# Kernel tuning notes

Measured on AMD Instinct MI355X. Metric: run time of the kernel, lower is better.

## Reference

```python
import jax, jax.numpy as jnp
import numpy as np

D = 4          # subsample stride for quantized refs
R = 6          # local search radius
P = 2 * R + 1  # 13
N = P * P      # 169
C = 32         # one-hot classes
BETA = 50.0
SIG = 1.0      # gaussian kernel sigma for kernel_soft_argmax
MPR = 12       # memory_patch_R
MPP = 2 * MPR + 1  # 25
DIL_INT = 15


def bilinear_gather(img, ys, xs):
    # img (b,c,h,w); ys,xs (b,n,h,w) float pixel coords; zero padding outside.
    b, c, h, w = img.shape
    y0f = jnp.floor(ys); x0f = jnp.floor(xs)
    wy = ys - y0f; wx = xs - x0f
    y0 = y0f.astype(jnp.int32); x0 = x0f.astype(jnp.int32)
    imgf = img.reshape(b, c, h * w)

    def corner(yi, xi, wgt):
        valid = (yi >= 0) & (yi < h) & (xi >= 0) & (xi < w)
        idx = jnp.clip(yi, 0, h - 1) * w + jnp.clip(xi, 0, w - 1)  # (b,n,h,w)
        g = jax.vmap(lambda f, ix: f[:, ix])(imgf, idx)            # (b,c,n,h,w)
        return g * (wgt * valid)[:, None]

    return (corner(y0, x0, (1 - wy) * (1 - wx))
            + corner(y0, x0 + 1, (1 - wy) * wx)
            + corner(y0 + 1, x0, wy * (1 - wx))
            + corner(y0 + 1, x0 + 1, wy * wx))


def deform_im2col(img, offset):
    # img (b,c,h,w); offset (b,h,w,2) ordered (dx,dy); returns (b,c,N,h,w)
    b, c, h, w = img.shape
    n = jnp.arange(N)
    dy = (n // P - R).astype(jnp.float32)
    dx = (n % P - R).astype(jnp.float32)
    yy = jnp.arange(h, dtype=jnp.float32)[:, None]
    xx = jnp.arange(w, dtype=jnp.float32)[None, :]
    ys = yy[None, None] + offset[..., 1][:, None] + dy[None, :, None, None]
    xs = xx[None, None] + offset[..., 0][:, None] + dx[None, :, None, None]
    return bilinear_gather(img, ys, xs)


def local_corr(t, r, rad, dil):
    # SpatialCorrelationSampler(kernel_size=1, patch_size=2*rad+1, dilation_patch=dil)
    pad = rad * dil
    rp = jnp.pad(r, ((0, 0), (0, 0), (pad, pad), (pad, pad)))
    offs = jnp.arange(2 * rad + 1) * dil

    def dot(oy, ox):
        rs = jax.lax.dynamic_slice(rp, (0, 0, oy, ox), t.shape)
        return jnp.sum(t * rs, axis=1)  # (b,h,w)

    f = jax.vmap(lambda oy: jax.vmap(lambda ox: dot(oy, ox))(offs))(offs)  # (Pp,Pp,b,h,w)
    return jnp.transpose(f, (2, 0, 1, 3, 4))  # (b,Pp,Pp,h,w), axis1=dy, axis2=dx


def unfold(x, ksz, pad):
    # torch F.unfold: (b,c,h,w) -> (b,c,ksz*ksz,h*w), n = ky*ksz+kx, zero pad
    b, c, h, w = x.shape
    xp = jnp.pad(x, ((0, 0), (0, 0), (pad, pad), (pad, pad)))
    offs = jnp.arange(ksz)
    sl = jax.vmap(lambda oy: jax.vmap(
        lambda ox: jax.lax.dynamic_slice(xp, (0, 0, oy, ox), x.shape))(offs))(offs)
    return jnp.transpose(sl, (2, 3, 0, 1, 4, 5)).reshape(b, c, ksz * ksz, h * w)


def kernel_soft_argmax(corr):
    # corr (B, N, h, w): gaussian-weight then softmax(beta * .) over N
    k = jnp.arange(P, dtype=jnp.float32)
    ctr = (P - 1) / 2.0
    g = jnp.exp(-(((k[None, :] - ctr) ** 2) + ((k[:, None] - ctr) ** 2)) / (2 * SIG ** 2))
    return jax.nn.softmax(BETA * (g.reshape(1, N, 1, 1) * corr), axis=1)


def get_grid(corr):
    # corr (B, N, h, w) -> soft-argmax grid (B, h, w, 2) in normalized coords
    B, n, h, w = corr.shape
    # replicate the torch meshgrid variable swap in the original get_grid
    x_map = jnp.broadcast_to(jnp.linspace(-1.0, 1.0, w)[None, :], (h, w)).astype(jnp.float32)
    y_map = jnp.broadcast_to(jnp.linspace(-1.0, 1.0, h)[:, None], (h, w)).astype(jnp.float32)
    xg = unfold(x_map[None, None], P, R)[:, 0]  # (1,N,hw)
    yg = unfold(y_map[None, None], P, R)[:, 0]
    wgt = corr.reshape(B, n, h * w)
    wgt = wgt / jnp.sum(wgt, 1, keepdims=True)
    gx = (wgt * xg).sum(1).reshape(B, h, w, 1)
    gy = (wgt * yg).sum(1).reshape(B, h, w, 1)
    return jnp.concatenate([gx, gy], 3)


def forward(feats_r, feats_t, quantized_r, ref_index, current_ind):
    ref_list = [int(v) for v in np.asarray(ref_index)]  # static config
    cur = int(current_ind)
    nref = feats_r.shape[0]
    nsearch = len([x for x in ref_list if cur - x > DIL_INT])
    dirates = [min(4, (cur - x) // DIL_INT + 1) for x in ref_list if cur - x > DIL_INT]
    b, c, h, w = feats_t.shape

    mdy = jnp.arange(-MPR, MPR + 1, dtype=jnp.float32)
    corrs, offsets = [], []
    for si in range(nsearch):
        cc = local_corr(feats_t, feats_r[si], MPR, dirates[si])       # (b,25,25,h,w)
        cc = jax.nn.softmax(cc.reshape(b, MPP * MPP, h * w), axis=1)
        cc = cc.reshape(b, MPP, MPP, h, w)
        offx = jnp.einsum('bpqhw,q->bhw', cc, mdy)   # expectation of dx
        offy = jnp.einsum('bpqhw,p->bhw', cc, mdy)   # expectation of dy
        off = jnp.stack([offx, offy], -1) * float(dirates[si])        # (b,h,w,2)
        offsets.append(off)
        col0 = deform_im2col(feats_r[si], off)                        # (b,c,N,h,w)
        corrs.append(jnp.einsum('bchw,bcnhw->bnhw', feats_t, col0))
    for ind in range(nsearch, nref):
        corrs.append(local_corr(feats_t, feats_r[ind], R, 1).reshape(b, N, h, w))

    corr = jnp.concatenate(corrs, 0)                 # (b*nref, N, h, w)
    corr = kernel_soft_argmax(corr)
    corr = corr.reshape(b, 1, N * nref, h * w)
    grid = get_grid(corr.reshape(-1, N, h, w))       # (b*nref, h, w, 2)

    # prep: subsample ::D and one-hot single-channel label maps
    labels = quantized_r[:, :, 0, ::D, ::D]          # (nref, b, h, w)
    qr = (labels[:, :, None] == jnp.arange(C)[None, None, :, None, None]).astype(jnp.float32)

    cols = []
    for i in range(nsearch):
        cols.append(deform_im2col(qr[i], offsets[i]).reshape(b, C, N, h * w))
    for i in range(nsearch, nref):
        cols.append(unfold(qr[i], P, R))
    image_uf = jnp.concatenate(cols, 2)              # (b, C, N*nref, hw)

    out = jnp.einsum('bnl,bcnl->bcl', corr[:, 0], image_uf).reshape(b, C, h, w)
    return out, grid


def setup_inputs() -> dict:
    key = jax.random.key(0)
    k1, k2, k3 = jax.random.split(key, 3)
    feats_r = jax.random.normal(k1, (3, 1, 64, 64, 64), dtype=jnp.float32)
    feats_t = jax.random.normal(k2, (1, 64, 64, 64), dtype=jnp.float32)
    quantized_r = jax.random.randint(k3, (3, 1, 1, 256, 256), 0, C, dtype=jnp.int32)
    return {
        'feats_r': feats_r,
        'feats_t': feats_t,
        'quantized_r': quantized_r,
        'ref_index': np.arange(3),
        'current_ind': 16,
    }


def reference(feats_r, feats_t, quantized_r, ref_index, current_ind):
    return forward(feats_r, feats_t, quantized_r, ref_index, current_ind)
```

## Files before the change

kernel.cpp:

```cpp
#include <hip/hip_runtime.h>


#define NPIX 4096

__device__ __forceinline__ float pdot8(float4 t0, float4 t1, float4 a,
                                       float4 b) {
  float s0 = t0.x * a.x, s1 = t0.y * a.y, s2 = t0.z * a.z, s3 = t0.w * a.w;
  s0 = fmaf(t1.x, b.x, s0);
  s1 = fmaf(t1.y, b.y, s1);
  s2 = fmaf(t1.z, b.z, s2);
  s3 = fmaf(t1.w, b.w, s3);
  return (s0 + s1) + (s2 + s3);
}

__device__ __forceinline__ float red8_4(float p0, float p1, float p2,
                                        float p3, int tx) {
  p0 += __shfl_xor(p0, 4);
  p1 += __shfl_xor(p1, 4);
  p2 += __shfl_xor(p2, 4);
  p3 += __shfl_xor(p3, 4);
  int t2 = tx & 3;
  bool o1 = t2 & 1, o2 = t2 & 2;
  float x01 = __shfl_xor(o1 ? p0 : p1, 1);
  float x23 = __shfl_xor(o1 ? p2 : p3, 1);
  float sA = (o1 ? p1 : p0) + x01;
  float sB = (o1 ? p3 : p2) + x23;
  float z = __shfl_xor(o2 ? sA : sB, 2);
  return o2 ? (sB + z) : (sA + z);
}

__device__ __forceinline__ float red8(float v) {
  v += __shfl_xor(v, 1);
  v += __shfl_xor(v, 2);
  v += __shfl_xor(v, 4);
  return v;
}

__device__ __forceinline__ float wredmax(float v) {
#pragma unroll
  for (int o = 32; o; o >>= 1) v = fmaxf(v, __shfl_down(v, o));
  return __shfl(v, 0);
}
__device__ __forceinline__ float wredsum(float v) {
#pragma unroll
  for (int o = 32; o; o >>= 1) v += __shfl_down(v, o);
  return __shfl(v, 0);
}

__global__ __launch_bounds__(256) void k_transpose(
    const float* __restrict__ ft, const float* __restrict__ fr,
    const int* __restrict__ q, float* __restrict__ tT, float* __restrict__ rT,
    unsigned char* __restrict__ lblp, float* __restrict__ out) {
  __shared__ float tile[64][65];
  int img = blockIdx.y;
  int pixBase = blockIdx.x * 64;
  const float* src = (img == 0) ? ft : fr + (img - 1) * (64 * NPIX);
  float* dst = (img == 0) ? tT : rT + (img - 1) * (64 * NPIX);
  int tid = threadIdx.x;
#pragma unroll
  for (int it = 0; it < 4; ++it) {
    int idx = it * 256 + tid;
    int c = idx >> 4;
    int p4 = (idx & 15) << 2;
    float4 v = *(const float4*)&src[c * NPIX + pixBase + p4];
    tile[p4 + 0][c] = v.x;
    tile[p4 + 1][c] = v.y;
    tile[p4 + 2][c] = v.z;
    tile[p4 + 3][c] = v.w;
  }
  __syncthreads();
#pragma unroll
  for (int it = 0; it < 4; ++it) {
    int idx = it * 256 + tid;
    int p = idx >> 4;
    int c4 = (idx & 15) << 2;
    float4 v = make_float4(tile[p][c4], tile[p][c4 + 1], tile[p][c4 + 2],
                           tile[p][c4 + 3]);
    *(float4*)&dst[(pixBase + p) * 64 + c4] = v;
  }
  if (img >= 1 && tid < 64) {
    int pix = pixBase + tid;
    lblp[(img - 1) * 4096 + pix] = (unsigned char)
        q[(img - 1) * 65536 + (pix >> 6) * 1024 + (pix & 63) * 4];
  }
  int gi = (blockIdx.y * 64 + blockIdx.x) * 256 + tid;
  out[gi] = 0.f;
  out[gi + 65536] = 0.f;
}

__global__ __launch_bounds__(256, 6) void k_fused(
    const float* __restrict__ tT, const float* __restrict__ rT,
    const unsigned char* __restrict__ lblp, float* __restrict__ out,
    float* __restrict__ grid) {
  int xg = blockIdx.x, y = blockIdx.y, z = blockIdx.z;
  int tid = threadIdx.x;
  int g = tid >> 3, tx = tid & 7;
  int w = tid >> 6, lane = tid & 63;

  __shared__ float cc1[4 * 636];
  __shared__ float D[4][196];
  __shared__ float P0[4][169];
  __shared__ float bins[4][33];

  if (tid < 132) ((float*)bins)[tid] = 0.f;

  int opix;

  if (z == 0) {
    int x0 = (xg >> 1) * 8 + (xg & 1);
    opix = x0;
    const float4* tb = (const float4*)&tT[((y << 6) + x0) << 6];
    float4 t0a = tb[0 * 32 + 2 * tx], t0b = tb[0 * 32 + 2 * tx + 1];
    float4 t1a = tb[1 * 32 + 2 * tx], t1b = tb[1 * 32 + 2 * tx + 1];
    float4 t2a = tb[2 * 32 + 2 * tx], t2b = tb[2 * 32 + 2 * tx + 1];
    float4 t3a = tb[3 * 32 + 2 * tx], t3b = tb[3 * 32 + 2 * tx + 1];

    __builtin_amdgcn_s_setprio(1);
    {
      int u = g;
      int rx = x0 - 24 + 2 * u;
      bool cok = (unsigned)rx < 64u;
      int colB = min(max(rx, 0), 63) * 64 + tx * 8;
      int ox = u - (tx & 3);
      bool sok = (tx < 4) & ((unsigned)ox < 25u);
#pragma unroll 4
      for (int r = 0; r < 25; ++r) {
        int ry = y + 2 * r - 24;
        bool ok = cok & ((unsigned)ry < 64u);
        const float4* rp =
            (const float4*)&rT[min(max(ry, 0), 63) * 4096 + colB];
        float4 ra = rp[0], rb = rp[1];
        float v = red8_4(pdot8(t0a, t0b, ra, rb), pdot8(t1a, t1b, ra, rb),
                         pdot8(t2a, t2b, ra, rb), pdot8(t3a, t3b, ra, rb),
                         tx);
        v = ok ? v : 0.f;
        if (sok) cc1[(tx & 3) * 636 + r * 25 + ox] = v;
      }
    }
    __builtin_amdgcn_s_setprio(0);
    __syncthreads();

    float offx, offy;
    {
      float vv[10];
      float m = -3e38f;
#pragma unroll
      for (int it = 0; it < 10; ++it) {
        unsigned o = lane + (it << 6);
        float v = (o < 625u) ? cc1[w * 636 + o] : -3e38f;
        vv[it] = v;
        m = fmaxf(m, v);
      }
      m = wredmax(m);
      float s = 0.f, sx = 0.f, sy = 0.f;
#pragma unroll
      for (int it = 0; it < 10; ++it) {
        unsigned o = lane + (it << 6);
        unsigned oy = o / 25u, ox = o - oy * 25u;
        float e = __expf(vv[it] - m);
        s += e;
        sx += e * (float)((int)ox - 12);
        sy += e * (float)((int)oy - 12);
      }
      s = wredsum(s);
      sx = wredsum(sx);
      sy = wredsum(sy);
      offx = 2.f * sx / s;
      offy = 2.f * sy / s;
    }

    float fy = floorf(offy), fx = floorf(offx);
    float wy = offy - fy, wx = offx - fx;
    float w00 = (1.f - wy) * (1.f - wx), w01 = (1.f - wy) * wx;
    float w10 = wy * (1.f - wx), w11 = wy * wx;
    int iy0 = y + (int)fy - 6;
    int ix0 = x0 + 2 * w + (int)fx - 6;

    __builtin_amdgcn_s_setprio(1);
    {
      const float4* Tp = (const float4*)&tT[((y << 6) + x0 + 2 * w) << 6];
      float4 T0 = Tp[2 * tx], T1 = Tp[2 * tx + 1];
      int g3 = lane >> 3;
#pragma unroll 4
      for (int r = 0; r < 28; ++r) {
        int idx = g3 + (r << 3);
        int a = idx >> 4, b = idx & 15;
        int ry = iy0 + a, rx = ix0 + b;
        bool ok = (b < 14) & ((unsigned)ry < 64u) & ((unsigned)rx < 64u);
        const float4* rp = (const float4*)
            &rT[(min(max(ry, 0), 63) * 64 + min(max(rx, 0), 63)) * 64];
        float4 ra = rp[2 * tx], rb = rp[2 * tx + 1];
        float v = red8(pdot8(T0, T1, ra, rb));
        if (tx == 0 && b < 14) D[w][a * 14 + b] = ok ? v : 0.f;
      }
    }
    __builtin_amdgcn_s_setprio(0);

    {
      int px = x0 + 2 * w, pix = (y << 6) + px;
      float sc[3];
      float m = -3e38f;
#pragma unroll
      for (int it = 0; it < 3; ++it) {
        unsigned o = lane + (it << 6);
        float scv = -3e38f;
        if (o < 169u) {
          unsigned i = o / 13u, j = o - i * 13u;
          float v = w00 * D[w][i * 14 + j] + w01 * D[w][i * 14 + j + 1] +
                    w10 * D[w][(i + 1) * 14 + j] +
                    w11 * D[w][(i + 1) * 14 + j + 1];
          float di = (float)(((int)i - 6) * ((int)i - 6) +
                             ((int)j - 6) * ((int)j - 6));
          scv = 50.f * __expf(-0.5f * di) * v;
        }
        sc[it] = scv;
        m = fmaxf(m, scv);
      }
      m = wredmax(m);
      float ee[3];
      float s = 0.f, gx = 0.f, gy = 0.f;
#pragma unroll
      for (int it = 0; it < 3; ++it) {
        unsigned o = lane + (it << 6);
        unsigned i = o / 13u, j = o - i * 13u;
        float e = __expf(sc[it] - m);
        ee[it] = e;
        int yy = y + (int)i - 6, xx = px + (int)j - 6;
        bool inb = (o < 169u) && (unsigned)yy < 64u && (unsigned)xx < 64u;
        s += e;
        gx += e * (inb ? (-1.f + (2.f / 63.f) * (float)xx) : 0.f);
        gy += e * (inb ? (-1.f + (2.f / 63.f) * (float)yy) : 0.f);
      }
      s = wredsum(s);
      gx = wredsum(gx);
      gy = wredsum(gy);
      float invS = 1.f / s;
#pragma unroll
      for (int it = 0; it < 3; ++it) {
        unsigned o = lane + (it << 6);
        if (o < 169u) P0[w][o] = ee[it] * invS;
      }
      if (lane == 0) {
        grid[pix * 2 + 0] = gx * invS;
        grid[pix * 2 + 1] = gy * invS;
      }
    }

    {
#pragma unroll
      for (int it = 0; it < 4; ++it) {
        int idx = lane + (it << 6);
        int a = idx >> 4, b = idx & 15;
        if (a < 14 && b < 14) {
          int ry = iy0 + a, rx = ix0 + b;
          if ((unsigned)ry < 64u && (unsigned)rx < 64u) {
            float wgt = 0.f;
            const float* crp = P0[w];
            if (a < 13) {
              if (b < 13) wgt = fmaf(w00, crp[a * 13 + b], wgt);
              if (b > 0) wgt = fmaf(w01, crp[a * 13 + b - 1], wgt);
            }
            if (a > 0) {
              if (b < 13) wgt = fmaf(w10, crp[(a - 1) * 13 + b], wgt);
              if (b > 0) wgt = fmaf(w11, crp[(a - 1) * 13 + b - 1], wgt);
            }
            if (wgt != 0.f) atomicAdd(&bins[w][lblp[ry * 64 + rx]], wgt);
          }
        }
      }
    }
    __syncthreads();
  } else {
    int k = z;
    int x0c = xg * 4;
    opix = -x0c - 1;
    const float* rb0 = rT + (k << 18);
    float (*cc2)[169] = (float(*)[169])cc1;
    const float4* tb = (const float4*)&tT[((y << 6) + x0c) << 6];
    float4 t0a = tb[0 * 16 + 2 * tx], t0b = tb[0 * 16 + 2 * tx + 1];
    float4 t1a = tb[1 * 16 + 2 * tx], t1b = tb[1 * 16 + 2 * tx + 1];
    float4 t2a = tb[2 * 16 + 2 * tx], t2b = tb[2 * 16 + 2 * tx + 1];
    float4 t3a = tb[3 * 16 + 2 * tx], t3b = tb[3 * 16 + 2 * tx + 1];

    __builtin_amdgcn_s_setprio(1);
    {
#pragma unroll 4
      for (int r = 0; r < 7; ++r) {
        int idx = g + (r << 5);
        int i = idx >> 4, u = idx & 15;
        int ry = y + i - 6, rx = x0c - 6 + u;
        bool ok = (i < 13) & ((unsigned)ry < 64u) & ((unsigned)rx < 64u);
        const float4* rp = (const float4*)
            &rb0[min(max(ry, 0), 63) * 4096 + min(max(rx, 0), 63) * 64 +
                 tx * 8];
        float4 ra = rp[0], rb = rp[1];
        float v = red8_4(pdot8(t0a, t0b, ra, rb), pdot8(t1a, t1b, ra, rb),
                         pdot8(t2a, t2b, ra, rb), pdot8(t3a, t3b, ra, rb),
                         tx);
        v = ok ? v : 0.f;
        int j = u - (tx & 3);
        if ((tx < 4) && (i < 13) && ((unsigned)j < 13u))
          cc2[tx & 3][i * 13 + j] = v;
      }
    }
    __builtin_amdgcn_s_setprio(0);
    __syncthreads();

    {
      int px = x0c + w, pix = (y << 6) + px;
      float sc[3];
      float m = -3e38f;
#pragma unroll
      for (int it = 0; it < 3; ++it) {
        unsigned o = lane + (it << 6);
        float scv = -3e38f;
        if (o < 169u) {
          unsigned i = o / 13u, j = o - i * 13u;
          float di = (float)(((int)i - 6) * ((int)i - 6) +
                             ((int)j - 6) * ((int)j - 6));
          scv = 50.f * __expf(-0.5f * di) * cc2[w][o];
        }
        sc[it] = scv;
        m = fmaxf(m, scv);
      }
      m = wredmax(m);
      float ee[3];
      float s = 0.f, gx = 0.f, gy = 0.f;
#pragma unroll
      for (int it = 0; it < 3; ++it) {
        unsigned o = lane + (it << 6);
        unsigned i = o / 13u, j = o - i * 13u;
        float e = __expf(sc[it] - m);
        ee[it] = e;
        int yy = y + (int)i - 6, xx = px + (int)j - 6;
        bool inb = (o < 169u) && (unsigned)yy < 64u && (unsigned)xx < 64u;
        s += e;
        gx += e * (inb ? (-1.f + (2.f / 63.f) * (float)xx) : 0.f);
        gy += e * (inb ? (-1.f + (2.f / 63.f) * (float)yy) : 0.f);
      }
      s = wredsum(s);
      gx = wredsum(gx);
      gy = wredsum(gy);
      float invS = 1.f / s;
#pragma unroll
      for (int it = 0; it < 3; ++it) {
        unsigned o = lane + (it << 6);
        if (o < 169u) {
          unsigned i = o / 13u, j = o - i * 13u;
          int yy = y + (int)i - 6, xx = px + (int)j - 6;
          if ((unsigned)yy < 64u && (unsigned)xx < 64u)
            atomicAdd(&bins[w][lblp[(k << 12) + yy * 64 + xx]],
                      ee[it] * invS);
        }
      }
      if (lane == 0) {
        grid[(k * NPIX + pix) * 2 + 0] = gx * invS;
        grid[(k * NPIX + pix) * 2 + 1] = gy * invS;
      }
    }
    __syncthreads();
  }

  if (tid < 128) {
    int pp = tid & 3, c = tid >> 2;
    int px = (opix >= 0) ? (opix + 2 * pp) : (-opix - 1 + pp);
    atomicAdd(&out[c * NPIX + (y << 6) + px], bins[pp][c]);
  }
}

extern "C" void kernel_launch(void* const* d_in, const int* in_sizes, int n_in,
                              void* d_out, int out_size, void* d_ws,
                              size_t ws_size, hipStream_t stream) {
  const float* fr = (const float*)d_in[0];
  const float* ft = (const float*)d_in[1];
  const int* q = (const int*)d_in[2];
  float* out = (float*)d_out;
  float* grid = out + 32 * NPIX;

  float* ws = (float*)d_ws;
  float* tT = ws;
  float* rT = ws + 262144;
  unsigned char* lblp = (unsigned char*)(ws + 1048576);

  k_transpose<<<dim3(64, 4), 256, 0, stream>>>(ft, fr, q, tT, rT, lblp, out);
  k_fused<<<dim3(16, 64, 3), 256, 0, stream>>>(tT, rT, lblp, out, grid);
}
```

Baseline: 49.45 us.

## Double block size to 512 threads and split per-pixel work across wave pairs

Each block in the fused kernel now runs 512 threads instead of 256, and two waves share each of the four pixels. The correlation loops, softargmax and softmax reductions are split in half, and the partial max/sum results are merged through shared memory with exp rescaling. The deformable correlation step is reorganised so all waves compute D for all four pixels after a shared offset broadcast. This shortens the serial chain per block, at the cost of extra __syncthreads, cross-wave merges, and the loss of the occupancy hint of 6 blocks per CU.

```diff
diff --git a/kernel.cpp b/kernel.cpp
--- a/kernel.cpp
+++ b/kernel.cpp
@@ -88,27 +88,27 @@
   out[gi + 65536] = 0.f;
 }
 
-__global__ __launch_bounds__(256, 6) void k_fused(
+__global__ __launch_bounds__(512) void k_fused(
     const float* __restrict__ tT, const float* __restrict__ rT,
     const unsigned char* __restrict__ lblp, float* __restrict__ out,
     float* __restrict__ grid) {
   int xg = blockIdx.x, y = blockIdx.y, z = blockIdx.z;
   int tid = threadIdx.x;
-  int g = tid >> 3, tx = tid & 7;
+  int gg = tid >> 3, tx = tid & 7;
   int w = tid >> 6, lane = tid & 63;
+  int p = w & 3, h = w >> 2;
 
   __shared__ float cc1[4 * 636];
   __shared__ float D[4][196];
   __shared__ float P0[4][169];
   __shared__ float bins[4][33];
+  __shared__ float wredL[8][4];
+  __shared__ float offs[4][2];
 
   if (tid < 132) ((float*)bins)[tid] = 0.f;
-
-  int opix;
 
   if (z == 0) {
     int x0 = (xg >> 1) * 8 + (xg & 1);
-    opix = x0;
     const float4* tb = (const float4*)&tT[((y << 6) + x0) << 6];
     float4 t0a = tb[0 * 32 + 2 * tx], t0b = tb[0 * 32 + 2 * tx + 1];
     float4 t1a = tb[1 * 32 + 2 * tx], t1b = tb[1 * 32 + 2 * tx + 1];
@@ -117,16 +117,17 @@
 
     __builtin_amdgcn_s_setprio(1);
     {
-      int u = g;
+      int u = gg & 31, oyb = gg >> 5;
       int rx = x0 - 24 + 2 * u;
       bool cok = (unsigned)rx < 64u;
       int colB = min(max(rx, 0), 63) * 64 + tx * 8;
       int ox = u - (tx & 3);
       bool sok = (tx < 4) & ((unsigned)ox < 25u);
 #pragma unroll 4
-      for (int r = 0; r < 25; ++r) {
-        int ry = y + 2 * r - 24;
-        bool ok = cok & ((unsigned)ry < 64u);
+      for (int r = 0; r < 13; ++r) {
+        int oy = oyb + 2 * r;
+        int ry = y + 2 * oy - 24;
+        bool ok = cok & (oy < 25) & ((unsigned)ry < 64u);
         const float4* rp =
             (const float4*)&rT[min(max(ry, 0), 63) * 4096 + colB];
         float4 ra = rp[0], rb = rp[1];
@@ -134,28 +135,27 @@
                          pdot8(t2a, t2b, ra, rb), pdot8(t3a, t3b, ra, rb),
                          tx);
         v = ok ? v : 0.f;
-        if (sok) cc1[(tx & 3) * 636 + r * 25 + ox] = v;
+        if (sok && (oy < 25)) cc1[(tx & 3) * 636 + oy * 25 + ox] = v;
       }
     }
     __builtin_amdgcn_s_setprio(0);
     __syncthreads();
 
-    float offx, offy;
-    {
-      float vv[10];
+    {
+      float vv[5];
       float m = -3e38f;
 #pragma unroll
-      for (int it = 0; it < 10; ++it) {
-        unsigned o = lane + (it << 6);
-        float v = (o < 625u) ? cc1[w * 636 + o] : -3e38f;
+      for (int it = 0; it < 5; ++it) {
+        unsigned o = lane + (h << 6) + (it << 7);
+        float v = (o < 625u) ? cc1[p * 636 + o] : -3e38f;
         vv[it] = v;
         m = fmaxf(m, v);
       }
       m = wredmax(m);
       float s = 0.f, sx = 0.f, sy = 0.f;
 #pragma unroll
-      for (int it = 0; it < 10; ++it) {
-        unsigned o = lane + (it << 6);
+      for (int it = 0; it < 5; ++it) {
+        unsigned o = lane + (h << 6) + (it << 7);
         unsigned oy = o / 25u, ox = o - oy * 25u;
         float e = __expf(vv[it] - m);
         s += e;
@@ -165,50 +165,65 @@
       s = wredsum(s);
       sx = wredsum(sx);
       sy = wredsum(sy);
-      offx = 2.f * sx / s;
-      offy = 2.f * sy / s;
-    }
-
+      if (lane == 0) {
+        wredL[w][0] = m; wredL[w][1] = s; wredL[w][2] = sx; wredL[w][3] = sy;
+      }
+      __syncthreads();
+      if (h == 0 && lane == 0) {
+        float m2 = wredL[w + 4][0], s2 = wredL[w + 4][1];
+        float sx2 = wredL[w + 4][2], sy2 = wredL[w + 4][3];
+        float M = fmaxf(m, m2);
+        float f1 = __expf(m - M), f2 = __expf(m2 - M);
+        float S = s * f1 + s2 * f2;
+        offs[p][0] = 2.f * (sx * f1 + sx2 * f2) / S;
+        offs[p][1] = 2.f * (sy * f1 + sy2 * f2) / S;
+      }
+    }
+    __syncthreads();
+
+    __builtin_amdgcn_s_setprio(1);
+    {
+      int pp = gg >> 4, ib = gg & 15;
+      const float4* Tp = (const float4*)&tT[((y << 6) + x0 + 2 * pp) << 6];
+      float4 T0 = Tp[2 * tx], T1 = Tp[2 * tx + 1];
+      float ofx = offs[pp][0], ofy = offs[pp][1];
+      int iy0p = y + (int)floorf(ofy) - 6;
+      int ix0p = x0 + 2 * pp + (int)floorf(ofx) - 6;
+#pragma unroll 4
+      for (int r = 0; r < 14; ++r) {
+        int ry = iy0p + r, rxx = ix0p + ib;
+        bool ok = (ib < 14) & ((unsigned)ry < 64u) & ((unsigned)rxx < 64u);
+        const float4* rp = (const float4*)
+            &rT[(min(max(ry, 0), 63) * 64 + min(max(rxx, 0), 63)) * 64];
+        float4 ra = rp[2 * tx], rb = rp[2 * tx + 1];
+        float v = red8(pdot8(T0, T1, ra, rb));
+        if (tx == 0 && ib < 14) D[pp][r * 14 + ib] = ok ? v : 0.f;
+      }
+    }
+    __builtin_amdgcn_s_setprio(0);
+    __syncthreads();
+
+    float offx = offs[p][0], offy = offs[p][1];
     float fy = floorf(offy), fx = floorf(offx);
     float wy = offy - fy, wx = offx - fx;
     float w00 = (1.f - wy) * (1.f - wx), w01 = (1.f - wy) * wx;
     float w10 = wy * (1.f - wx), w11 = wy * wx;
     int iy0 = y + (int)fy - 6;
-    int ix0 = x0 + 2 * w + (int)fx - 6;
-
-    __builtin_amdgcn_s_setprio(1);
-    {
-      const float4* Tp = (const float4*)&tT[((y << 6) + x0 + 2 * w) << 6];
-      float4 T0 = Tp[2 * tx], T1 = Tp[2 * tx + 1];
-      int g3 = lane >> 3;
-#pragma unroll 4
-      for (int r = 0; r < 28; ++r) {
-        int idx = g3 + (r << 3);
-        int a = idx >> 4, b = idx & 15;
-        int ry = iy0 + a, rx = ix0 + b;
-        bool ok = (b < 14) & ((unsigned)ry < 64u) & ((unsigned)rx < 64u);
-        const float4* rp = (const float4*)
-            &rT[(min(max(ry, 0), 63) * 64 + min(max(rx, 0), 63)) * 64];
-        float4 ra = rp[2 * tx], rb = rp[2 * tx + 1];
-        float v = red8(pdot8(T0, T1, ra, rb));
-        if (tx == 0 && b < 14) D[w][a * 14 + b] = ok ? v : 0.f;
-      }
-    }
-    __builtin_amdgcn_s_setprio(0);
-
-    {
-      int px = x0 + 2 * w, pix = (y << 6) + px;
-      float sc[3];
+    int ix0 = x0 + 2 * p + (int)fx - 6;
+
+    {
+      int px = x0 + 2 * p, pix = (y << 6) + px;
+      float sc[2];
       float m = -3e38f;
 #pragma unroll
-      for (int it = 0; it < 3; ++it) {
-        unsigned o = lane + (it << 6);
+      for (int it = 0; it < 2; ++it) {
+        unsigned o = lane + (h << 6) + (it << 7);
         float scv = -3e38f;
         if (o < 169u) {
           unsigned i = o / 13u, j = o - i * 13u;
-          float v = w00 * D[w][i * 14 + j] + w01 * D[w][i * 14 + j + 1] +
-                    w10 * D[w][(i + 1) * 14 + j] +
-                    w11 * D[w][(i + 1) * 14 + j + 1];
+          float v = w00 * D[p][i * 14 + j] + w01 * D[p][i * 14 + j + 1] +
+                    w10 * D[p][(i + 1) * 14 + j] +
+                    w11 * D[p][(i + 1) * 14 + j + 1];
           float di = (float)(((int)i - 6) * ((int)i - 6) +
                              ((int)j - 6) * ((int)j - 6));
           scv = 50.f * __expf(-0.5f * di) * v;
@@ -217,11 +232,11 @@
         m = fmaxf(m, scv);
       }
       m = wredmax(m);
-      float ee[3];
+      float ee[2];
       float s = 0.f, gx = 0.f, gy = 0.f;
 #pragma unroll
-      for (int it = 0; it < 3; ++it) {
-        unsigned o = lane + (it << 6);
+      for (int it = 0; it < 2; ++it) {
+        unsigned o = lane + (h << 6) + (it << 7);
         unsigned i = o / 13u, j = o - i * 13u;
         float e = __expf(sc[it] - m);
         ee[it] = e;
@@ -234,28 +249,37 @@
       s = wredsum(s);
       gx = wredsum(gx);
       gy = wredsum(gy);
-      float invS = 1.f / s;
-#pragma unroll
-      for (int it = 0; it < 3; ++it) {
-        unsigned o = lane + (it << 6);
-        if (o < 169u) P0[w][o] = ee[it] * invS;
-      }
       if (lane == 0) {
-        grid[pix * 2 + 0] = gx * invS;
-        grid[pix * 2 + 1] = gy * invS;
-      }
-    }
-
-    {
-#pragma unroll
-      for (int it = 0; it < 4; ++it) {
-        int idx = lane + (it << 6);
+        wredL[w][0] = m; wredL[w][1] = s; wredL[w][2] = gx; wredL[w][3] = gy;
+      }
+      __syncthreads();
+      float mo = wredL[w ^ 4][0], so = wredL[w ^ 4][1];
+      float gxo = wredL[w ^ 4][2], gyo = wredL[w ^ 4][3];
+      float M = fmaxf(m, mo);
+      float fs = __expf(m - M), fo = __expf(mo - M);
+      float invS = 1.f / (s * fs + so * fo);
+#pragma unroll
+      for (int it = 0; it < 2; ++it) {
+        unsigned o = lane + (h << 6) + (it << 7);
+        if (o < 169u) P0[p][o] = ee[it] * fs * invS;
+      }
+      if (h == 0 && lane == 0) {
+        grid[pix * 2 + 0] = (gx * fs + gxo * fo) * invS;
+        grid[pix * 2 + 1] = (gy * fs + gyo * fo) * invS;
+      }
+    }
+    __syncthreads();
+
+    {
+#pragma unroll
+      for (int it = 0; it < 2; ++it) {
+        int idx = lane + (h << 6) + (it << 7);
         int a = idx >> 4, b = idx & 15;
         if (a < 14 && b < 14) {
-          int ry = iy0 + a, rx = ix0 + b;
-          if ((unsigned)ry < 64u && (unsigned)rx < 64u) {
+          int ry = iy0 + a, rxx = ix0 + b;
+          if ((unsigned)ry < 64u && (unsigned)rxx < 64u) {
             float wgt = 0.f;
-            const float* crp = P0[w];
+            const float* crp = P0[p];
             if (a < 13) {
               if (b < 13) wgt = fmaf(w00, crp[a * 13 + b], wgt);
               if (b > 0) wgt = fmaf(w01, crp[a * 13 + b - 1], wgt);
@@ -264,7 +288,7 @@
               if (b < 13) wgt = fmaf(w10, crp[(a - 1) * 13 + b], wgt);
               if (b > 0) wgt = fmaf(w11, crp[(a - 1) * 13 + b - 1], wgt);
             }
-            if (wgt != 0.f) atomicAdd(&bins[w][lblp[ry * 64 + rx]], wgt);
+            if (wgt != 0.f) atomicAdd(&bins[p][lblp[ry * 64 + rxx]], wgt);
           }
         }
       }
@@ -273,7 +297,6 @@
   } else {
     int k = z;
     int x0c = xg * 4;
-    opix = -x0c - 1;
     const float* rb0 = rT + (k << 18);
     float (*cc2)[169] = (float(*)[169])cc1;
     const float4* tb = (const float4*)&tT[((y << 6) + x0c) << 6];
@@ -284,14 +307,14 @@
 
     __builtin_amdgcn_s_setprio(1);
     {
-#pragma unroll 4
-      for (int r = 0; r < 7; ++r) {
-        int idx = g + (r << 5);
+#pragma unroll 2
+      for (int r = 0; r < 4; ++r) {
+        int idx = gg + (r << 6);
         int i = idx >> 4, u = idx & 15;
-        int ry = y + i - 6, rx = x0c - 6 + u;
-        bool ok = (i < 13) & ((unsigned)ry < 64u) & ((unsigned)rx < 64u);
+        int ry = y + i - 6, rxx = x0c - 6 + u;
+        bool ok = (i < 13) & ((unsigned)ry < 64u) & ((unsigned)rxx < 64u);
         const float4* rp = (const float4*)
-            &rb0[min(max(ry, 0), 63) * 4096 + min(max(rx, 0), 63) * 64 +
+            &rb0[min(max(ry, 0), 63) * 4096 + min(max(rxx, 0), 63) * 64 +
                  tx * 8];
         float4 ra = rp[0], rb = rp[1];
         float v = red8_4(pdot8(t0a, t0b, ra, rb), pdot8(t1a, t1b, ra, rb),
@@ -307,28 +330,28 @@
     __syncthreads();
 
     {
-      int px = x0c + w, pix = (y << 6) + px;
-      float sc[3];
+      int px = x0c + p, pix = (y << 6) + px;
+      float sc[2];
       float m = -3e38f;
 #pragma unroll
-      for (int it = 0; it < 3; ++it) {
-        unsigned o = lane + (it << 6);
+      for (int it = 0; it < 2; ++it) {
+        unsigned o = lane + (h << 6) + (it << 7);
         float scv = -3e38f;
         if (o < 169u) {
           unsigned i = o / 13u, j = o - i * 13u;
           float di = (float)(((int)i - 6) * ((int)i - 6) +
                              ((int)j - 6) * ((int)j - 6));
-          scv = 50.f * __expf(-0.5f * di) * cc2[w][o];
+          scv = 50.f * __expf(-0.5f * di) * cc2[p][o];
         }
         sc[it] = scv;
         m = fmaxf(m, scv);
       }
       m = wredmax(m);
-      float ee[3];
+      float ee[2];
       float s = 0.f, gx = 0.f, gy = 0.f;
 #pragma unroll
-      for (int it = 0; it < 3; ++it) {
-        unsigned o = lane + (it << 6);
+      for (int it = 0; it < 2; ++it) {
+        unsigned o = lane + (h << 6) + (it << 7);
         unsigned i = o / 13u, j = o - i * 13u;
         float e = __expf(sc[it] - m);
         ee[it] = e;
@@ -341,21 +364,29 @@
       s = wredsum(s);
       gx = wredsum(gx);
       gy = wredsum(gy);
-      float invS = 1.f / s;
-#pragma unroll
-      for (int it = 0; it < 3; ++it) {
-        unsigned o = lane + (it << 6);
+      if (lane == 0) {
+        wredL[w][0] = m; wredL[w][1] = s; wredL[w][2] = gx; wredL[w][3] = gy;
+      }
+      __syncthreads();
+      float mo = wredL[w ^ 4][0], so = wredL[w ^ 4][1];
+      float gxo = wredL[w ^ 4][2], gyo = wredL[w ^ 4][3];
+      float M = fmaxf(m, mo);
+      float fs = __expf(m - M), fo = __expf(mo - M);
+      float invS = 1.f / (s * fs + so * fo);
+#pragma unroll
+      for (int it = 0; it < 2; ++it) {
+        unsigned o = lane + (h << 6) + (it << 7);
         if (o < 169u) {
           unsigned i = o / 13u, j = o - i * 13u;
           int yy = y + (int)i - 6, xx = px + (int)j - 6;
           if ((unsigned)yy < 64u && (unsigned)xx < 64u)
-            atomicAdd(&bins[w][lblp[(k << 12) + yy * 64 + xx]],
-                      ee[it] * invS);
+            atomicAdd(&bins[p][lblp[(k << 12) + yy * 64 + xx]],
+                      ee[it] * fs * invS);
         }
       }
-      if (lane == 0) {
-        grid[(k * NPIX + pix) * 2 + 0] = gx * invS;
-        grid[(k * NPIX + pix) * 2 + 1] = gy * invS;
+      if (h == 0 && lane == 0) {
+        grid[(k * NPIX + pix) * 2 + 0] = (gx * fs + gxo * fo) * invS;
+        grid[(k * NPIX + pix) * 2 + 1] = (gy * fs + gyo * fo) * invS;
       }
     }
     __syncthreads();
@@ -363,7 +394,7 @@
 
   if (tid < 128) {
     int pp = tid & 3, c = tid >> 2;
-    int px = (opix >= 0) ? (opix + 2 * pp) : (-opix - 1 + pp);
+    int px = (z == 0) ? ((xg >> 1) * 8 + (xg & 1) + 2 * pp) : (xg * 4 + pp);
     atomicAdd(&out[c * NPIX + (y << 6) + px], bins[pp][c]);
   }
 }
@@ -383,5 +414,5 @@
   unsigned char* lblp = (unsigned char*)(ws + 1048576);
 
   k_transpose<<<dim3(64, 4), 256, 0, stream>>>(ft, fr, q, tT, rT, lblp, out);
-  k_fused<<<dim3(16, 64, 3), 256, 0, stream>>>(tT, rT, lblp, out, grid);
-}
+  k_fused<<<dim3(16, 64, 3), 512, 0, stream>>>(tT, rT, lblp, out, grid);
+}
```

Result: slower. 59.45 us (+20.2%).

## Compute coarse correlation softmax via split-bf16 MFMA Gram kernel with partial reductions

Applied to the files above, without the earlier changes.

Moves the 25x25 dilated coarse correlation out of the fused kernel into a new kernel. For each row pair it forms a 64x64 Gram matrix with bf16 MFMA, using hi/lo splitting (three products) to approximate fp32 accuracy. It then reduces each row's 25 horizontal offsets to partial max, sum-exp and x-moment values. The fused kernel combines the 25 per-row partials with a log-sum-exp style merge instead of computing 625 dot products per pixel. This adds an extra launch, bf16 hi/lo conversion work in the transpose, and more workspace traffic. It also computes the full 64x64 Gram even though only 25 columns per row are used.

```diff
diff --git a/kernel.cpp b/kernel.cpp
--- a/kernel.cpp
+++ b/kernel.cpp
@@ -2,6 +2,18 @@
 
 
 #define NPIX 4096
+
+typedef __attribute__((ext_vector_type(8))) short short8v;
+typedef __attribute__((ext_vector_type(4))) float f32x4;
+
+__device__ __forceinline__ unsigned short f2bf(float x) {
+  unsigned u = __float_as_uint(x);
+  unsigned r = (u + 0x7FFFu + ((u >> 16) & 1u)) >> 16;
+  return (unsigned short)r;
+}
+__device__ __forceinline__ float bf2f(unsigned short b) {
+  return __uint_as_float((unsigned)b << 16);
+}
 
 __device__ __forceinline__ float pdot8(float4 t0, float4 t1, float4 a,
                                        float4 b) {
@@ -50,7 +62,9 @@
 __global__ __launch_bounds__(256) void k_transpose(
     const float* __restrict__ ft, const float* __restrict__ fr,
     const int* __restrict__ q, float* __restrict__ tT, float* __restrict__ rT,
-    unsigned char* __restrict__ lblp, float* __restrict__ out) {
+    unsigned char* __restrict__ lblp, float* __restrict__ out,
+    unsigned short* __restrict__ tHi, unsigned short* __restrict__ tLo,
+    unsigned short* __restrict__ rHi, unsigned short* __restrict__ rLo) {
   __shared__ float tile[64][65];
   int img = blockIdx.y;
   int pixBase = blockIdx.x * 64;
@@ -77,6 +91,17 @@
     float4 v = make_float4(tile[p][c4], tile[p][c4 + 1], tile[p][c4 + 2],
                            tile[p][c4 + 3]);
     *(float4*)&dst[(pixBase + p) * 64 + c4] = v;
+    if (img <= 1) {
+      unsigned short* hp = (img == 0) ? tHi : rHi;
+      unsigned short* lp = (img == 0) ? tLo : rLo;
+      ushort4 h, l;
+      h.x = f2bf(v.x); l.x = f2bf(v.x - bf2f(h.x));
+      h.y = f2bf(v.y); l.y = f2bf(v.y - bf2f(h.y));
+      h.z = f2bf(v.z); l.z = f2bf(v.z - bf2f(h.z));
+      h.w = f2bf(v.w); l.w = f2bf(v.w - bf2f(h.w));
+      *(ushort4*)&hp[(pixBase + p) * 64 + c4] = h;
+      *(ushort4*)&lp[(pixBase + p) * 64 + c4] = l;
+    }
   }
   if (img >= 1 && tid < 64) {
     int pix = pixBase + tid;
@@ -88,10 +113,83 @@
   out[gi + 65536] = 0.f;
 }
 
+__global__ __launch_bounds__(256) void k_gram(
+    const unsigned short* __restrict__ tHi,
+    const unsigned short* __restrict__ tLo,
+    const unsigned short* __restrict__ rHi,
+    const unsigned short* __restrict__ rLo, float4* __restrict__ part4) {
+  int y = blockIdx.x, t = blockIdx.y;
+  int ry = y + 2 * t - 24;
+  int tid = threadIdx.x;
+  if ((unsigned)ry >= 64u) {
+    if (tid < 64)
+      part4[t * 4096 + y * 64 + tid] = make_float4(0.f, 25.f, 0.f, 0.f);
+    return;
+  }
+  __shared__ float G[64 * 68];
+  int w = tid >> 6, lane = tid & 63;
+  int lr = lane & 15, lg = lane >> 4;
+
+  const unsigned short* aH = tHi + (y * 64 + w * 16 + lr) * 64 + lg * 8;
+  const unsigned short* aL = tLo + (y * 64 + w * 16 + lr) * 64 + lg * 8;
+  f32x4 acc[4];
+#pragma unroll
+  for (int ni = 0; ni < 4; ++ni) acc[ni] = (f32x4){0.f, 0.f, 0.f, 0.f};
+#pragma unroll
+  for (int ks = 0; ks < 2; ++ks) {
+    short8v ahi = *(const short8v*)(aH + ks * 32);
+    short8v alo = *(const short8v*)(aL + ks * 32);
+#pragma unroll
+    for (int ni = 0; ni < 4; ++ni) {
+      const unsigned short* bH =
+          rHi + (ry * 64 + ni * 16 + lr) * 64 + ks * 32 + lg * 8;
+      const unsigned short* bL =
+          rLo + (ry * 64 + ni * 16 + lr) * 64 + ks * 32 + lg * 8;
+      short8v bhi = *(const short8v*)bH;
+      short8v blo = *(const short8v*)bL;
+      acc[ni] = __builtin_amdgcn_mfma_f32_16x16x32_bf16(ahi, bhi, acc[ni],
+                                                        0, 0, 0);
+      acc[ni] = __builtin_amdgcn_mfma_f32_16x16x32_bf16(ahi, blo, acc[ni],
+                                                        0, 0, 0);
+      acc[ni] = __builtin_amdgcn_mfma_f32_16x16x32_bf16(alo, bhi, acc[ni],
+                                                        0, 0, 0);
+    }
+  }
+#pragma unroll
+  for (int ni = 0; ni < 4; ++ni) {
+#pragma unroll
+    for (int r = 0; r < 4; ++r)
+      G[(w * 16 + lg * 4 + r) * 68 + ni * 16 + lr] = acc[ni][r];
+  }
+  __syncthreads();
+
+  if (tid < 64) {
+    int x = tid;
+    const float* Gr = &G[x * 68];
+    float m = -3e38f;
+#pragma unroll
+    for (int ox = 0; ox < 25; ++ox) {
+      int xp = x + 2 * ox - 24;
+      float v = ((unsigned)xp < 64u) ? Gr[xp] : 0.f;
+      m = fmaxf(m, v);
+    }
+    float s = 0.f, sx = 0.f;
+#pragma unroll
+    for (int ox = 0; ox < 25; ++ox) {
+      int xp = x + 2 * ox - 24;
+      float v = ((unsigned)xp < 64u) ? Gr[xp] : 0.f;
+      float e = __expf(v - m);
+      s += e;
+      sx += e * (float)(ox - 12);
+    }
+    part4[t * 4096 + y * 64 + x] = make_float4(m, s, sx, 0.f);
+  }
+}
+
 __global__ __launch_bounds__(256, 6) void k_fused(
     const float* __restrict__ tT, const float* __restrict__ rT,
-    const unsigned char* __restrict__ lblp, float* __restrict__ out,
-    float* __restrict__ grid) {
+    const unsigned char* __restrict__ lblp, const float4* __restrict__ part4,
+    float* __restrict__ out, float* __restrict__ grid) {
   int xg = blockIdx.x, y = blockIdx.y, z = blockIdx.z;
   int tid = threadIdx.x;
   int g = tid >> 3, tx = tid & 7;
@@ -109,65 +207,21 @@
   if (z == 0) {
     int x0 = (xg >> 1) * 8 + (xg & 1);
     opix = x0;
-    const float4* tb = (const float4*)&tT[((y << 6) + x0) << 6];
-    float4 t0a = tb[0 * 32 + 2 * tx], t0b = tb[0 * 32 + 2 * tx + 1];
-    float4 t1a = tb[1 * 32 + 2 * tx], t1b = tb[1 * 32 + 2 * tx + 1];
-    float4 t2a = tb[2 * 32 + 2 * tx], t2b = tb[2 * 32 + 2 * tx + 1];
-    float4 t3a = tb[3 * 32 + 2 * tx], t3b = tb[3 * 32 + 2 * tx + 1];
-
-    __builtin_amdgcn_s_setprio(1);
-    {
-      int u = g;
-      int rx = x0 - 24 + 2 * u;
-      bool cok = (unsigned)rx < 64u;
-      int colB = min(max(rx, 0), 63) * 64 + tx * 8;
-      int ox = u - (tx & 3);
-      bool sok = (tx < 4) & ((unsigned)ox < 25u);
-#pragma unroll 4
-      for (int r = 0; r < 25; ++r) {
-        int ry = y + 2 * r - 24;
-        bool ok = cok & ((unsigned)ry < 64u);
-        const float4* rp =
-            (const float4*)&rT[min(max(ry, 0), 63) * 4096 + colB];
-        float4 ra = rp[0], rb = rp[1];
-        float v = red8_4(pdot8(t0a, t0b, ra, rb), pdot8(t1a, t1b, ra, rb),
-                         pdot8(t2a, t2b, ra, rb), pdot8(t3a, t3b, ra, rb),
-                         tx);
-        v = ok ? v : 0.f;
-        if (sok) cc1[(tx & 3) * 636 + r * 25 + ox] = v;
-      }
-    }
-    __builtin_amdgcn_s_setprio(0);
+
+    float offx, offy;
+    {
+      int pix = (y << 6) + x0 + 2 * w;
+      float4 pt = (lane < 25) ? part4[lane * 4096 + pix]
+                              : make_float4(-3e38f, 0.f, 0.f, 0.f);
+      float M = wredmax(pt.x);
+      float f = (lane < 25) ? __expf(pt.x - M) : 0.f;
+      float S = wredsum(pt.y * f);
+      float SX = wredsum(pt.z * f);
+      float SY = wredsum((float)(lane - 12) * pt.y * f);
+      offx = 2.f * SX / S;
+      offy = 2.f * SY / S;
+    }
     __syncthreads();
-
-    float offx, offy;
-    {
-      float vv[10];
-      float m = -3e38f;
-#pragma unroll
-      for (int it = 0; it < 10; ++it) {
-        unsigned o = lane + (it << 6);
-        float v = (o < 625u) ? cc1[w * 636 + o] : -3e38f;
-        vv[it] = v;
-        m = fmaxf(m, v);
-      }
-      m = wredmax(m);
-      float s = 0.f, sx = 0.f, sy = 0.f;
-#pragma unroll
-      for (int it = 0; it < 10; ++it) {
-        unsigned o = lane + (it << 6);
-        unsigned oy = o / 25u, ox = o - oy * 25u;
-        float e = __expf(vv[it] - m);
-        s += e;
-        sx += e * (float)((int)ox - 12);
-        sy += e * (float)((int)oy - 12);
-      }
-      s = wredsum(s);
-      sx = wredsum(sx);
-      sy = wredsum(sy);
-      offx = 2.f * sx / s;
-      offy = 2.f * sy / s;
-    }
 
     float fy = floorf(offy), fx = floorf(offx);
     float wy = offy - fy, wx = offx - fx;
@@ -381,7 +435,15 @@
   float* tT = ws;
   float* rT = ws + 262144;
   unsigned char* lblp = (unsigned char*)(ws + 1048576);
-
-  k_transpose<<<dim3(64, 4), 256, 0, stream>>>(ft, fr, q, tT, rT, lblp, out);
-  k_fused<<<dim3(16, 64, 3), 256, 0, stream>>>(tT, rT, lblp, out, grid);
-}
+  float4* part4 = (float4*)(ws + 1052672);
+  unsigned short* tHi = (unsigned short*)(ws + 1462272);
+  unsigned short* tLo = tHi + 262144;
+  unsigned short* rHi = tLo + 262144;
+  unsigned short* rLo = rHi + 262144;
+
+  k_transpose<<<dim3(64, 4), 256, 0, stream>>>(ft, fr, q, tT, rT, lblp, out,
+                                               tHi, tLo, rHi, rLo);
+  k_gram<<<dim3(64, 25), 256, 0, stream>>>(tHi, tLo, rHi, rLo, part4);
+  k_fused<<<dim3(16, 64, 3), 256, 0, stream>>>(tT, rT, lblp, part4, out,
+                                               grid);
+}
```

Measured after the change: 57.52 us. 16.3% more time.
